# Performance work log

Hardware: AMD Instinct MI355X
Metric: run time of the kernel (lower is better)

## Reference

```python
import jax, jax.numpy as jnp
import numpy as np

TWO_PI = 2.0 * np.pi
HID, FREQ, OUT = 64, 10, 16
BS, T, K, D = 1024, 128, 8, 32
IN_DIM = K * D


def hard_sigmoid(x):
    # torch.nn.Hardsigmoid: clip(x/6 + 1/2, 0, 1)
    return jnp.clip(x / 6.0 + 0.5, 0.0, 1.0)


def setup_inputs() -> dict:
    key = jax.random.key(0)
    ks = jax.random.split(key, 16)
    s_in = 1.0 / np.sqrt(IN_DIM)
    s_h = 1.0 / np.sqrt(HID)
    inp = {
        "g1": jax.random.normal(ks[0], (BS, T, K, D), jnp.float32),
        "W_i": jax.random.normal(ks[1], (IN_DIM, HID), jnp.float32) * s_in,
        "U_i": jax.random.normal(ks[2], (HID, HID), jnp.float32) * s_h,
        "b_i": jnp.zeros((HID,), jnp.float32),
        "W_ste": jax.random.normal(ks[3], (IN_DIM, HID), jnp.float32) * s_in,
        "U_ste": jax.random.normal(ks[4], (HID, HID), jnp.float32) * s_h,
        "b_ste": jnp.ones((HID,), jnp.float32),
        "W_fre": jax.random.normal(ks[5], (IN_DIM, FREQ), jnp.float32) * s_in,
        "U_fre": jax.random.normal(ks[6], (HID, FREQ), jnp.float32) * s_h,
        "b_fre": jnp.ones((FREQ,), jnp.float32),
        "W_c": jax.random.normal(ks[7], (IN_DIM, HID), jnp.float32) * s_in,
        "U_c": jax.random.normal(ks[8], (HID, HID), jnp.float32) * s_h,
        "b_c": jnp.zeros((HID,), jnp.float32),
        "W_o": jax.random.normal(ks[9], (IN_DIM, HID), jnp.float32) * s_in,
        "U_o": jax.random.normal(ks[10], (HID, HID), jnp.float32) * s_h,
        "b_o": jnp.zeros((HID,), jnp.float32),
        "U_a": jax.random.normal(ks[11], (FREQ, 1), jnp.float32) / np.sqrt(FREQ),
        "b_a": jnp.zeros((HID,), jnp.float32),
        "W_p": jax.random.normal(ks[12], (HID, OUT), jnp.float32) * s_h,
        "b_p": jnp.zeros((OUT,), jnp.float32),
        "fc_w": jax.random.normal(ks[13], (OUT, 1), jnp.float32) / np.sqrt(OUT),
        "fc_b": jnp.zeros((1,), jnp.float32),
    }
    return inp


def reference(g1, W_i, U_i, b_i, W_ste, U_ste, b_ste, W_fre, U_fre, b_fre,
              W_c, U_c, b_c, W_o, U_o, b_o, U_a, b_a, W_p, b_p, fc_w, fc_b):
    bs, Tn, k, d = g1.shape
    x_seq = g1.reshape(bs, Tn, k * d).transpose(1, 0, 2)  # (T, bs, IN)
    H, F = U_i.shape[0], U_fre.shape[1]
    freq = jnp.arange(F, dtype=g1.dtype) / F                 # frequency vector
    h0 = jnp.zeros((bs, H), g1.dtype)
    S0 = jnp.zeros((bs, H, F), g1.dtype)
    times = jnp.arange(1, Tn + 1, dtype=g1.dtype)            # time = t+1 per step

    def step(carry, inp):
        h, S_re, S_im = carry
        x, t = inp
        i = hard_sigmoid(x @ W_i + b_i + h @ U_i)
        ste = hard_sigmoid(x @ W_ste + b_ste + h @ U_ste)    # (bs,H)
        fre = hard_sigmoid(x @ W_fre + b_fre + h @ U_fre)    # (bs,F)
        f = ste[:, :, None] * fre[:, None, :]                # (bs,H,F)
        c = i * jnp.tanh(x @ W_c + b_c + h @ U_c)            # (bs,H)
        omega = TWO_PI * t * freq                            # (F,)
        S_re = f * S_re + c[:, :, None] * jnp.cos(omega)
        S_im = f * S_im + c[:, :, None] * jnp.sin(omega)
        A = S_re * S_re + S_im * S_im                        # (bs,H,F)
        a = jnp.tanh(jnp.einsum('bhf,f->bh', A, U_a[:, 0]) + b_a)
        o = hard_sigmoid(x @ W_o + b_o + h @ U_o)
        return (o * a, S_re, S_im), None

    (hT, _, _), _ = jax.lax.scan(step, (h0, S0, S0), (x_seq, times))
    p = hT @ W_p + b_p                                       # (bs, OUT)
    return p @ fc_w + fc_b                                   # pred: (bs, 1)
```

## Files before the change

kernel.cpp:

```cpp
#include <hip/hip_runtime.h>
#include <cstdint>

#define TSTEPS  128
#define INDIM   256
#define HIDDEN  64
#define FREQN   10
#define NOUT    16
#define XSTRIDE 272
#define NTILE   17

typedef __attribute__((ext_vector_type(8))) short bf16x8;
typedef __attribute__((ext_vector_type(4))) float f32x4;
typedef _Float16 f16;
typedef __attribute__((ext_vector_type(2))) _Float16 f16x2;

__device__ __forceinline__ unsigned short bf16h(float x) {
    unsigned u = __float_as_uint(x);
    return (unsigned short)((u + 0x7FFFu + ((u >> 16) & 1u)) >> 16);
}
__device__ __forceinline__ float rdlane(float v, int l) {
    return __int_as_float(__builtin_amdgcn_readlane(__float_as_int(v), l));
}
__device__ __forceinline__ float hsig(float x) {
    return fminf(fmaxf(__fmaf_rn(x, (1.0f / 6.0f), 0.5f), 0.0f), 1.0f);
}
__device__ __forceinline__ float tanh_f(float x) {
    float e = __expf(2.0f * x);
    return 1.0f - 2.0f / (e + 1.0f);
}
__device__ __forceinline__ float fdot2(f16x2 a, f16x2 b, float c) {
#if __has_builtin(__builtin_amdgcn_fdot2)
    return __builtin_amdgcn_fdot2(a, b, c, false);
#else
    return __fmaf_rn((float)a.x, (float)b.x, __fmaf_rn((float)a.y, (float)b.y, c));
#endif
}

__global__ void pack_w(const float* __restrict__ Wi, const float* __restrict__ Wst,
                       const float* __restrict__ Wc, const float* __restrict__ Wo,
                       const float* __restrict__ Wfr,
                       const float* __restrict__ bi, const float* __restrict__ bst,
                       const float* __restrict__ bc, const float* __restrict__ bo,
                       const float* __restrict__ bfr,
                       unsigned short* __restrict__ Wpk, float* __restrict__ bias)
{
    int idx = blockIdx.x * 256 + threadIdx.x;
    if (idx < 8 * NTILE * 64) {
        int l = idx & 63;
        int t = (idx >> 6) % NTILE;
        int s = idx / (64 * NTILE);
        int n = t * 16 + (l & 15);
        unsigned short* dst = Wpk + (size_t)idx * 16;
        #pragma unroll
        for (int i = 0; i < 8; ++i) {
            int k = s * 32 + (l >> 4) * 8 + i;
            float v;
            if      (n < 64)  v = Wi [k * 64 + n];
            else if (n < 128) v = Wst[k * 64 + (n - 64)];
            else if (n < 192) v = Wc [k * 64 + (n - 128)];
            else if (n < 256) v = Wo [k * 64 + (n - 192)];
            else if (n < 266) v = Wfr[k * 10 + (n - 256)];
            else              v = 0.f;
            unsigned short h = bf16h(v);
            float hf = __uint_as_float((unsigned)h << 16);
            dst[i]     = h;
            dst[8 + i] = bf16h(v - hf);
        }
    } else if (idx < 8 * NTILE * 64 + XSTRIDE) {
        int n = idx - 8 * NTILE * 64;
        float b;
        if      (n < 64)  b = bi [n];
        else if (n < 128) b = bst[n - 64];
        else if (n < 192) b = bc [n - 128];
        else if (n < 256) b = bo [n - 192];
        else if (n < 266) b = bfr[n - 256];
        else              b = 0.f;
        bias[n] = b;
    }
}

__global__ __launch_bounds__(256, 2)
void gemm_mfma(const float* __restrict__ A, const unsigned short* __restrict__ Wpk,
               const float* __restrict__ bias, float* __restrict__ outp,
               int ci, int tclog)
{
    const int tid = threadIdx.x;
    const int w   = tid >> 6, l = tid & 63;
    const int l15 = l & 15,  lg = l >> 4;
    const int tcm = (1 << tclog) - 1;
    const int rbase = blockIdx.x * 128 + w * 32;

    f32x4 acc[2][NTILE];
    #pragma unroll
    for (int rt = 0; rt < 2; ++rt)
        #pragma unroll
        for (int t = 0; t < NTILE; ++t) acc[rt][t] = (f32x4){0.f, 0.f, 0.f, 0.f};

    #pragma unroll
    for (int s = 0; s < 8; ++s) {
        bf16x8 ahi[2], alo[2];
        #pragma unroll
        for (int rt = 0; rt < 2; ++rt) {
            int rp   = rbase + rt * 16 + l15;
            int grow = ((rp >> tclog) << 7) + (ci << tclog) + (rp & tcm);
            const float* ap = A + (size_t)grow * INDIM + s * 32 + lg * 8;
            float4 a0 = *reinterpret_cast<const float4*>(ap);
            float4 a1 = *reinterpret_cast<const float4*>(ap + 4);
            float av[8] = {a0.x, a0.y, a0.z, a0.w, a1.x, a1.y, a1.z, a1.w};
            union { bf16x8 v; unsigned short u[8]; } H, L;
            #pragma unroll
            for (int i = 0; i < 8; ++i) {
                unsigned short h = bf16h(av[i]);
                H.u[i] = h;
                L.u[i] = bf16h(av[i] - __uint_as_float((unsigned)h << 16));
            }
            ahi[rt] = H.v; alo[rt] = L.v;
        }
        #pragma unroll
        for (int t = 0; t < NTILE; ++t) {
            const bf16x8* bp =
                reinterpret_cast<const bf16x8*>(Wpk + ((size_t)(s * NTILE + t) * 64 + l) * 16);
            bf16x8 bhi = bp[0], blo = bp[1];
            #pragma unroll
            for (int rt = 0; rt < 2; ++rt) {
                acc[rt][t] = __builtin_amdgcn_mfma_f32_16x16x32_bf16(ahi[rt], bhi, acc[rt][t], 0, 0, 0);
                acc[rt][t] = __builtin_amdgcn_mfma_f32_16x16x32_bf16(ahi[rt], blo, acc[rt][t], 0, 0, 0);
                acc[rt][t] = __builtin_amdgcn_mfma_f32_16x16x32_bf16(alo[rt], bhi, acc[rt][t], 0, 0, 0);
            }
        }
    }
    #pragma unroll
    for (int t = 0; t < NTILE; ++t) {
        float bv = bias[t * 16 + l15];
        #pragma unroll
        for (int rt = 0; rt < 2; ++rt) {
            int rp0 = rbase + rt * 16 + lg * 4;
            #pragma unroll
            for (int r = 0; r < 4; ++r)
                outp[(size_t)(rp0 + r) * XSTRIDE + t * 16 + l15] = acc[rt][t][r] + bv;
        }
    }
}

__global__ void cstab_kernel(float2* __restrict__ tab)
{
    int idx = blockIdx.x * 256 + threadIdx.x;
    if (idx >= TSTEPS * FREQN) return;
    int t = idx / FREQN, j = idx - t * FREQN;
    float time = (float)(t + 1);
    float om = (6.28318530717958647692f * time) * ((float)j / 10.0f);
    float s, c;
    sincosf(om, &s, &c);
    tab[idx] = make_float2(c, s);
}

__global__ __launch_bounds__(256, 1)
void rec_kernel(const float* __restrict__ xproj,
                const float* __restrict__ Ui, const float* __restrict__ Us,
                const float* __restrict__ Uc, const float* __restrict__ Uo,
                const float* __restrict__ Ufre, const float* __restrict__ Ua,
                const float* __restrict__ ba,
                const float* __restrict__ csTab,
                float* __restrict__ state,
                const float* __restrict__ Wp, const float* __restrict__ bp,
                const float* __restrict__ fcw, const float* __restrict__ fcb,
                float* __restrict__ outv,
                int ci, int TC, int nchunks)
{
    __shared__ __align__(16) unsigned hx[4][32];
    const int tid  = threadIdx.x;
    const int lane = tid & 63, w = tid >> 6;
    const int row  = blockIdx.x * 4 + w;
    const int jc   = (lane < FREQN) ? lane : (FREQN - 1);

    f16x2 Uk[32][4];
    f16x2 Uf2[32];
    #pragma unroll
    for (int m = 0; m < 32; ++m) {
        int ka = 2 * m, kb = 2 * m + 1;
        Uk[m][0] = (f16x2){(f16)Ui[ka * 64 + lane], (f16)Ui[kb * 64 + lane]};
        Uk[m][1] = (f16x2){(f16)Us[ka * 64 + lane], (f16)Us[kb * 64 + lane]};
        Uk[m][2] = (f16x2){(f16)Uc[ka * 64 + lane], (f16)Uc[kb * 64 + lane]};
        Uk[m][3] = (f16x2){(f16)Uo[ka * 64 + lane], (f16)Uo[kb * 64 + lane]};
        Uf2[m]   = (f16x2){(f16)Ufre[ka * FREQN + jc], (f16)Ufre[kb * FREQN + jc]};
    }

    float hv;
    float Sre[FREQN], Sim[FREQN];
    if (ci == 0) {
        hv = 0.f;
        #pragma unroll
        for (int j = 0; j < FREQN; ++j) { Sre[j] = 0.f; Sim[j] = 0.f; }
    } else {
        hv = state[row * 64 + lane];
        #pragma unroll
        for (int j = 0; j < FREQN; ++j) {
            Sre[j] = state[65536 + j * 65536 + row * 64 + lane];
            Sim[j] = state[65536 + 655360 + j * 65536 + row * 64 + lane];
        }
    }

    const float ba_l = ba[lane];
    float sua[FREQN];
    #pragma unroll
    for (int j = 0; j < FREQN; ++j) sua[j] = Ua[j];

    {
        float hb = __shfl_down(hv, 1, 64);
        f16x2 hp; hp.x = (f16)hv; hp.y = (f16)hb;
        if (!(lane & 1)) hx[w][lane >> 1] = __builtin_bit_cast(unsigned, hp);
    }

    const float* xb = xproj + (size_t)row * TC * XSTRIDE;
    float xi = xb[lane], xs = xb[64 + lane], xc = xb[128 + lane];
    float xo = xb[192 + lane], xf = xb[256 + jc];

    for (int tt = 0; tt < TC; ++tt) {
        unsigned hw_[32];
        #pragma unroll
        for (int m = 0; m < 32; ++m) hw_[m] = hx[w][m];

        float ai = 0.f, as_ = 0.f, ac = 0.f, ao = 0.f, af = 0.f;
        #pragma unroll
        for (int m = 0; m < 32; ++m) {
            f16x2 h2 = __builtin_bit_cast(f16x2, hw_[m]);
            ai  = fdot2(h2, Uk[m][0], ai);
            as_ = fdot2(h2, Uk[m][1], as_);
            ac  = fdot2(h2, Uk[m][2], ac);
            ao  = fdot2(h2, Uk[m][3], ao);
            af  = fdot2(h2, Uf2[m],  af);
        }

        float cxi = xi, cxs = xs, cxc = xc, cxo = xo, cxf = xf;
        if (tt + 1 < TC) {
            const float* b2 = xb + (size_t)(tt + 1) * XSTRIDE;
            xi = b2[lane]; xs = b2[64 + lane]; xc = b2[128 + lane];
            xo = b2[192 + lane]; xf = b2[256 + jc];
        }
        const float* cs = csTab + (size_t)(ci * TC + tt) * (2 * FREQN);

        float gi = hsig(cxi + ai);
        float gs = hsig(cxs + as_);
        float go = hsig(cxo + ao);
        float gc = gi * tanh_f(cxc + ac);
        float freh = hsig(cxf + af);
        float aacc = 0.f;
        #pragma unroll
        for (int j = 0; j < FREQN; ++j) {
            float fre = rdlane(freh, j);
            float cj = cs[2 * j];
            float sj = cs[2 * j + 1];
            float fj = gs * fre;
            Sre[j] = __fmaf_rn(fj, Sre[j], gc * cj);
            Sim[j] = __fmaf_rn(fj, Sim[j], gc * sj);
            float Aj = __fmaf_rn(Sre[j], Sre[j], Sim[j] * Sim[j]);
            aacc = __fmaf_rn(Aj, sua[j], aacc);
        }
        hv = go * tanh_f(aacc + ba_l);

        float hb = __shfl_down(hv, 1, 64);
        f16x2 hp; hp.x = (f16)hv; hp.y = (f16)hb;
        if (!(lane & 1)) hx[w][lane >> 1] = __builtin_bit_cast(unsigned, hp);
    }

    if (ci == nchunks - 1) {
        float wef = 0.f;
        #pragma unroll
        for (int o = 0; o < NOUT; ++o)
            wef = __fmaf_rn(Wp[lane * NOUT + o], fcw[o], wef);
        float v = hv * wef;
        #pragma unroll
        for (int off = 32; off > 0; off >>= 1) v += __shfl_xor(v, off, 64);
        if (lane == 0) {
            float cb = fcb[0];
            #pragma unroll
            for (int o = 0; o < NOUT; ++o) cb = __fmaf_rn(bp[o], fcw[o], cb);
            outv[row] = v + cb;
        }
    } else {
        state[row * 64 + lane] = hv;
        #pragma unroll
        for (int j = 0; j < FREQN; ++j) {
            state[65536 + j * 65536 + row * 64 + lane] = Sre[j];
            state[65536 + 655360 + j * 65536 + row * 64 + lane] = Sim[j];
        }
    }
}

extern "C" void kernel_launch(void* const* d_in, const int* in_sizes, int n_in,
                              void* d_out, int out_size, void* d_ws, size_t ws_size,
                              hipStream_t stream)
{
    const float* g1  = (const float*)d_in[0];
    const float* Wi  = (const float*)d_in[1];
    const float* Ui  = (const float*)d_in[2];
    const float* bi  = (const float*)d_in[3];
    const float* Wst = (const float*)d_in[4];
    const float* Ust = (const float*)d_in[5];
    const float* bst = (const float*)d_in[6];
    const float* Wfr = (const float*)d_in[7];
    const float* Ufq = (const float*)d_in[8];
    const float* bfr = (const float*)d_in[9];
    const float* Wc  = (const float*)d_in[10];
    const float* Uc  = (const float*)d_in[11];
    const float* bc  = (const float*)d_in[12];
    const float* Wo  = (const float*)d_in[13];
    const float* Uo  = (const float*)d_in[14];
    const float* bo  = (const float*)d_in[15];
    const float* Ua  = (const float*)d_in[16];
    const float* ba  = (const float*)d_in[17];
    const float* Wp  = (const float*)d_in[18];
    const float* bp  = (const float*)d_in[19];
    const float* fcw = (const float*)d_in[20];
    const float* fcb = (const float*)d_in[21];
    float* outv = (float*)d_out;

    const size_t stateFloats = 65536 + 2 * 655360;
    const size_t csFloats    = TSTEPS * FREQN * 2;
    const size_t wpkShorts   = (size_t)8 * NTILE * 64 * 16;
    int TC = 128;
    while (TC > 8 &&
           ((size_t)1024 * TC * XSTRIDE + stateFloats + csFloats + XSTRIDE) * 4
               + wpkShorts * 2 > ws_size)
        TC >>= 1;
    int tclog = 31 - __builtin_clz((unsigned)TC);
    int nchunks = TSTEPS / TC;

    float*  xproj = (float*)d_ws;
    float*  state = xproj + (size_t)1024 * TC * XSTRIDE;
    float*  csTab = state + stateFloats;
    float*  bias  = csTab + csFloats;
    unsigned short* Wpk = (unsigned short*)(bias + XSTRIDE);

    pack_w<<<36, 256, 0, stream>>>(Wi, Wst, Wc, Wo, Wfr, bi, bst, bc, bo, bfr, Wpk, bias);
    cstab_kernel<<<(TSTEPS * FREQN + 255) / 256, 256, 0, stream>>>((float2*)csTab);

    const int Mt = (1024 * TC) / 128;
    for (int ci = 0; ci < nchunks; ++ci) {
        gemm_mfma<<<Mt, 256, 0, stream>>>(g1, Wpk, bias, xproj, ci, tclog);
        rec_kernel<<<256, 256, 0, stream>>>(xproj, Ui, Ust, Uc, Uo, Ufq, Ua, ba,
                                            csTab, state, Wp, bp, fcw, fcb, outv,
                                            ci, TC, nchunks);
    }
}
```

Measured before the change: 479.0 us.

## Use MFMA for recurrent matvec and stage GEMM weights in LDS

```diff
diff --git a/kernel.cpp b/kernel.cpp
--- a/kernel.cpp
+++ b/kernel.cpp
@@ -8,11 +8,13 @@
 #define NOUT    16
 #define XSTRIDE 272
 #define NTILE   17
+#define SLICE   17408
 
 typedef __attribute__((ext_vector_type(8))) short bf16x8;
+typedef __attribute__((ext_vector_type(8))) unsigned short ushort8;
 typedef __attribute__((ext_vector_type(4))) float f32x4;
 typedef _Float16 f16;
-typedef __attribute__((ext_vector_type(2))) _Float16 f16x2;
+typedef __attribute__((ext_vector_type(8))) _Float16 f16x8;
 
 __device__ __forceinline__ unsigned short bf16h(float x) {
     unsigned u = __float_as_uint(x);
@@ -28,12 +30,14 @@
     float e = __expf(2.0f * x);
     return 1.0f - 2.0f / (e + 1.0f);
 }
-__device__ __forceinline__ float fdot2(f16x2 a, f16x2 b, float c) {
-#if __has_builtin(__builtin_amdgcn_fdot2)
-    return __builtin_amdgcn_fdot2(a, b, c, false);
-#else
-    return __fmaf_rn((float)a.x, (float)b.x, __fmaf_rn((float)a.y, (float)b.y, c));
-#endif
+__device__ __forceinline__ unsigned packf16(float a, float b) {
+    unsigned short la = __builtin_bit_cast(unsigned short, (f16)a);
+    unsigned short lb = __builtin_bit_cast(unsigned short, (f16)b);
+    return (unsigned)la | ((unsigned)lb << 16);
+}
+__device__ __forceinline__ void gload_lds16(const void* g, void* l) {
+    __builtin_amdgcn_global_load_lds((const __attribute__((address_space(1))) void*)g,
+                                     (__attribute__((address_space(3))) void*)l, 16, 0, 0);
 }
 
 __global__ void pack_w(const float* __restrict__ Wi, const float* __restrict__ Wst,
@@ -84,6 +88,7 @@
                const float* __restrict__ bias, float* __restrict__ outp,
                int ci, int tclog)
 {
+    extern __shared__ short Bsh[];
     const int tid = threadIdx.x;
     const int w   = tid >> 6, l = tid & 63;
     const int l15 = l & 15,  lg = l >> 4;
@@ -97,7 +102,25 @@
         for (int t = 0; t < NTILE; ++t) acc[rt][t] = (f32x4){0.f, 0.f, 0.f, 0.f};
 
     #pragma unroll
+    for (int u = 0; u < 9; ++u) {
+        int e = u * 256 + tid;
+        if (e < 2176)
+            gload_lds16(Wpk + (size_t)e * 8, &Bsh[e * 8]);
+    }
+    __syncthreads();
+
+    #pragma unroll
     for (int s = 0; s < 8; ++s) {
+        if (s + 1 < 8) {
+            const unsigned short* src = Wpk + (size_t)(s + 1) * SLICE;
+            short* dst = &Bsh[((s + 1) & 1) * SLICE];
+            #pragma unroll
+            for (int u = 0; u < 9; ++u) {
+                int e = u * 256 + tid;
+                if (e < 2176)
+                    gload_lds16(src + (size_t)e * 8, dst + e * 8);
+            }
+        }
         bf16x8 ahi[2], alo[2];
         #pragma unroll
         for (int rt = 0; rt < 2; ++rt) {
@@ -116,10 +139,10 @@
             }
             ahi[rt] = H.v; alo[rt] = L.v;
         }
+        const short* buf = &Bsh[(s & 1) * SLICE];
         #pragma unroll
         for (int t = 0; t < NTILE; ++t) {
-            const bf16x8* bp =
-                reinterpret_cast<const bf16x8*>(Wpk + ((size_t)(s * NTILE + t) * 64 + l) * 16);
+            const bf16x8* bp = reinterpret_cast<const bf16x8*>(buf + (t * 64 + l) * 16);
             bf16x8 bhi = bp[0], blo = bp[1];
             #pragma unroll
             for (int rt = 0; rt < 2; ++rt) {
@@ -128,6 +151,7 @@
                 acc[rt][t] = __builtin_amdgcn_mfma_f32_16x16x32_bf16(alo[rt], bhi, acc[rt][t], 0, 0, 0);
             }
         }
+        __syncthreads();
     }
     #pragma unroll
     for (int t = 0; t < NTILE; ++t) {
@@ -154,7 +178,7 @@
     tab[idx] = make_float2(c, s);
 }
 
-__global__ __launch_bounds__(256, 1)
+__global__ __launch_bounds__(64, 1)
 void rec_kernel(const float* __restrict__ xproj,
                 const float* __restrict__ Ui, const float* __restrict__ Us,
                 const float* __restrict__ Uc, const float* __restrict__ Uo,
@@ -167,22 +191,34 @@
                 float* __restrict__ outv,
                 int ci, int TC, int nchunks)
 {
-    __shared__ __align__(16) unsigned hx[4][32];
-    const int tid  = threadIdx.x;
-    const int lane = tid & 63, w = tid >> 6;
-    const int row  = blockIdx.x * 4 + w;
+    __shared__ float rowbuf[XSTRIDE];
+    __shared__ unsigned h2[32];
+    const int lane = threadIdx.x;
+    const int row  = blockIdx.x;
+    const int l15  = lane & 15, lg = lane >> 4;
     const int jc   = (lane < FREQN) ? lane : (FREQN - 1);
 
-    f16x2 Uk[32][4];
-    f16x2 Uf2[32];
-    #pragma unroll
-    for (int m = 0; m < 32; ++m) {
-        int ka = 2 * m, kb = 2 * m + 1;
-        Uk[m][0] = (f16x2){(f16)Ui[ka * 64 + lane], (f16)Ui[kb * 64 + lane]};
-        Uk[m][1] = (f16x2){(f16)Us[ka * 64 + lane], (f16)Us[kb * 64 + lane]};
-        Uk[m][2] = (f16x2){(f16)Uc[ka * 64 + lane], (f16)Uc[kb * 64 + lane]};
-        Uk[m][3] = (f16x2){(f16)Uo[ka * 64 + lane], (f16)Uo[kb * 64 + lane]};
-        Uf2[m]   = (f16x2){(f16)Ufre[ka * FREQN + jc], (f16)Ufre[kb * FREQN + jc]};
+    f16x8 Bf[NTILE][2];
+    #pragma unroll
+    for (int t = 0; t < NTILE; ++t) {
+        #pragma unroll
+        for (int kap = 0; kap < 2; ++kap) {
+            union { f16x8 v; f16 e[8]; } u;
+            #pragma unroll
+            for (int i = 0; i < 8; ++i) {
+                int k = kap * 32 + lg * 8 + i;
+                int n = t * 16 + l15;
+                float v;
+                if      (n < 64)  v = Ui [k * 64 + n];
+                else if (n < 128) v = Us [k * 64 + (n - 64)];
+                else if (n < 192) v = Uc [k * 64 + (n - 128)];
+                else if (n < 256) v = Uo [k * 64 + (n - 192)];
+                else if (n < 266) v = Ufre[k * 10 + (n - 256)];
+                else              v = 0.f;
+                u.e[i] = (f16)v;
+            }
+            Bf[t][kap] = u.v;
+        }
     }
 
     float hv;
@@ -207,8 +243,8 @@
 
     {
         float hb = __shfl_down(hv, 1, 64);
-        f16x2 hp; hp.x = (f16)hv; hp.y = (f16)hb;
-        if (!(lane & 1)) hx[w][lane >> 1] = __builtin_bit_cast(unsigned, hp);
+        unsigned d = packf16(hv, hb);
+        if (!(lane & 1)) h2[lane >> 1] = d;
     }
 
     const float* xb = xproj + (size_t)row * TC * XSTRIDE;
@@ -216,20 +252,22 @@
     float xo = xb[192 + lane], xf = xb[256 + jc];
 
     for (int tt = 0; tt < TC; ++tt) {
-        unsigned hw_[32];
-        #pragma unroll
-        for (int m = 0; m < 32; ++m) hw_[m] = hx[w][m];
-
-        float ai = 0.f, as_ = 0.f, ac = 0.f, ao = 0.f, af = 0.f;
-        #pragma unroll
-        for (int m = 0; m < 32; ++m) {
-            f16x2 h2 = __builtin_bit_cast(f16x2, hw_[m]);
-            ai  = fdot2(h2, Uk[m][0], ai);
-            as_ = fdot2(h2, Uk[m][1], as_);
-            ac  = fdot2(h2, Uk[m][2], ac);
-            ao  = fdot2(h2, Uk[m][3], ao);
-            af  = fdot2(h2, Uf2[m],  af);
-        }
+        f16x8 a0 = *reinterpret_cast<const f16x8*>((const char*)h2 + lg * 16);
+        f16x8 a1 = *reinterpret_cast<const f16x8*>((const char*)h2 + 64 + lg * 16);
+
+        #pragma unroll
+        for (int t = 0; t < NTILE; ++t) {
+            f32x4 z = (f32x4){0.f, 0.f, 0.f, 0.f};
+            z = __builtin_amdgcn_mfma_f32_16x16x32_f16(a0, Bf[t][0], z, 0, 0, 0);
+            z = __builtin_amdgcn_mfma_f32_16x16x32_f16(a1, Bf[t][1], z, 0, 0, 0);
+            if (lane < 16) rowbuf[t * 16 + lane] = z[0];
+        }
+
+        float si = rowbuf[lane];
+        float ss = rowbuf[64 + lane];
+        float sc = rowbuf[128 + lane];
+        float so = rowbuf[192 + lane];
+        float pfr = rowbuf[256 + jc];
 
         float cxi = xi, cxs = xs, cxc = xc, cxo = xo, cxf = xf;
         if (tt + 1 < TC) {
@@ -239,11 +277,11 @@
         }
         const float* cs = csTab + (size_t)(ci * TC + tt) * (2 * FREQN);
 
-        float gi = hsig(cxi + ai);
-        float gs = hsig(cxs + as_);
-        float go = hsig(cxo + ao);
-        float gc = gi * tanh_f(cxc + ac);
-        float freh = hsig(cxf + af);
+        float gi = hsig(cxi + si);
+        float gs = hsig(cxs + ss);
+        float go = hsig(cxo + so);
+        float gc = gi * tanh_f(cxc + sc);
+        float freh = hsig(cxf + pfr);
         float aacc = 0.f;
         #pragma unroll
         for (int j = 0; j < FREQN; ++j) {
@@ -259,8 +297,8 @@
         hv = go * tanh_f(aacc + ba_l);
 
         float hb = __shfl_down(hv, 1, 64);
-        f16x2 hp; hp.x = (f16)hv; hp.y = (f16)hb;
-        if (!(lane & 1)) hx[w][lane >> 1] = __builtin_bit_cast(unsigned, hp);
+        unsigned d = packf16(hv, hb);
+        if (!(lane & 1)) h2[lane >> 1] = d;
     }
 
     if (ci == nchunks - 1) {
@@ -332,13 +370,16 @@
     float*  bias  = csTab + csFloats;
     unsigned short* Wpk = (unsigned short*)(bias + XSTRIDE);
 
+    hipFuncSetAttribute((const void*)gemm_mfma,
+                        hipFuncAttributeMaxDynamicSharedMemorySize, 69632);
+
     pack_w<<<36, 256, 0, stream>>>(Wi, Wst, Wc, Wo, Wfr, bi, bst, bc, bo, bfr, Wpk, bias);
     cstab_kernel<<<(TSTEPS * FREQN + 255) / 256, 256, 0, stream>>>((float2*)csTab);
 
     const int Mt = (1024 * TC) / 128;
     for (int ci = 0; ci < nchunks; ++ci) {
-        gemm_mfma<<<Mt, 256, 0, stream>>>(g1, Wpk, bias, xproj, ci, tclog);
-        rec_kernel<<<256, 256, 0, stream>>>(xproj, Ui, Ust, Uc, Uo, Ufq, Ua, ba,
+        gemm_mfma<<<Mt, 256, 69632, stream>>>(g1, Wpk, bias, xproj, ci, tclog);
+        rec_kernel<<<1024, 64, 0, stream>>>(xproj, Ui, Ust, Uc, Uo, Ufq, Ua, ba,
                                             csTab, state, Wp, bp, fcw, fcb, outv,
                                             ci, TC, nchunks);
     }
```

Result: faster. 457.5 us (-4.5%).
